# Kernel optimization log

Hardware: AMD Instinct MI355X
Metric: run time of the kernel (lower is better)

## Reference

```python
import jax, jax.numpy as jnp
import numpy as np

# Per-type input feature dims (NODE_DIM values); max dim = 128 = padded width of x.
NODE_DIMS = np.array([16, 32, 64, 128, 64, 32, 16, 128], dtype=np.int32)
N_TYPES = 8
MAX_DIM = 128
FEAT = 256          # node_feature_dim
N_GRAPHS = 100000   # batch_size; one node of each type per graph


def setup_inputs() -> dict:
    key = jax.random.key(0)
    k1, k2, k3 = jax.random.split(key, 3)
    num_nodes = N_GRAPHS * N_TYPES
    x = jax.random.normal(k1, (num_nodes, MAX_DIM), dtype=jnp.float32)
    # Per-type Linear weights, padded to MAX_DIM on the input axis.
    W = jax.random.normal(k2, (N_TYPES, FEAT, MAX_DIM), dtype=jnp.float32) * 0.05
    b = jax.random.normal(k3, (N_TYPES, FEAT), dtype=jnp.float32) * 0.05
    return {"x": x, "W": W, "b": b}


def reference(x, W, b):
    # Node n = g*N_TYPES + k is the type-k node of graph g (the gather index
    # ptr[b] + node_name.index(k) in the original). Dropout is eval-mode (identity).
    # Mask weight columns beyond each type's true input dim: equivalent to
    # slicing x[:, :NODE_DIM[k]] before the per-type Linear.
    mask = (jnp.arange(MAX_DIM)[None, None, :] < jnp.asarray(NODE_DIMS)[:, None, None]).astype(x.dtype)  # [T,1,D]
    W_eff = W * mask  # [T,F,D]
    xg = x.reshape(N_GRAPHS, N_TYPES, MAX_DIM)  # [G,T,D]
    y = jnp.einsum("gtd,tfd->gtf", xg, W_eff) + b[None, :, :]  # [G,T,F]
    return y.reshape(N_GRAPHS * N_TYPES, FEAT)
```

## Files before the change

kernel.cpp:

```cpp
#include <hip/hip_runtime.h>
#include <hip/hip_bf16.h>

#define N_GRAPHS 100000
#define NTYPES 8
#define MAXD 128
#define FEAT 256
#define ROWS 64

typedef __attribute__((ext_vector_type(8))) short short8;
typedef __attribute__((ext_vector_type(4))) float f32x4;
typedef __attribute__((ext_vector_type(4))) unsigned uint4v;

constexpr int DIMS[NTYPES] = {16, 32, 64, 128, 64, 32, 16, 128};

__device__ __forceinline__ unsigned f2bf_u(float f) {
    unsigned u = __builtin_bit_cast(unsigned, f);
    return (u + 0x7fffu + ((u >> 16) & 1u)) >> 16;
}
__device__ __forceinline__ unsigned cvt2(float lo, float hi) {
    return f2bf_u(lo) | (f2bf_u(hi) << 16);
}
__device__ __forceinline__ short8 cvt8(f32x4 a, f32x4 b) {
    uint4v u;
    u.x = cvt2(a.x, a.y); u.y = cvt2(a.z, a.w);
    u.z = cvt2(b.x, b.y); u.w = cvt2(b.z, b.w);
    return __builtin_bit_cast(short8, u);
}

__global__ __launch_bounds__(256)
void prepack_w(const float* __restrict__ W, short8* __restrict__ wp)
{
    const int idx  = blockIdx.x * 256 + threadIdx.x;
    const int c16  = idx & 15;
    const int cgrp = (idx >> 4) & 3;
    const int ks   = (idx >> 6) & 3;
    const int nt   = (idx >> 8) & 3;
    const int wb   = (idx >> 10) & 3;
    const int t    = (idx >> 12) & 7;
    const int col  = wb * 64 + nt * 16 + c16;
    const int k    = ks * 32 + cgrp * 8;
    const int dim  = 16 << ((0x30123210u >> (4 * t)) & 0xf);
    const float* src = W + ((size_t)t * FEAT + col) * MAXD + k;
    f32x4 a = *(const f32x4*)src;
    f32x4 b = *(const f32x4*)(src + 4);
    #pragma unroll
    for (int j = 0; j < 4; ++j) {
        if (k + j     >= dim) a[j] = 0.f;
        if (k + 4 + j >= dim) b[j] = 0.f;
    }
    wp[idx] = cvt8(a, b);
}

template<int K32>
__device__ __forceinline__ void stage_tile(const float* __restrict__ x, int grow0, int t,
                                           unsigned short (* __restrict__ As)[136], int tid)
{
    constexpr int TPR    = K32 / 8;
    constexpr int RPP    = 256 / TPR;
    constexpr int PASSES = ROWS / RPP;
    const int rloc = tid / TPR;
    const int kg   = tid % TPR;
    #pragma unroll
    for (int p = 0; p < PASSES; ++p) {
        const int i = p * RPP + rloc;
        int g = grow0 + i;
        if (g >= N_GRAPHS) g = N_GRAPHS - 1;
        const float* rp = x + ((size_t)g * NTYPES + t) * MAXD + kg * 8;
        f32x4 v0 = __builtin_nontemporal_load((const f32x4*)rp);
        f32x4 v1 = __builtin_nontemporal_load((const f32x4*)rp + 1);
        *(short8*)&As[i][kg * 8] = cvt8(v0, v1);
    }
}

template<int T, bool PRE>
__device__ __forceinline__ void type_step(const float* __restrict__ x,
                                          const float* __restrict__ W,
                                          const float* __restrict__ bias_g,
                                          float* __restrict__ out,
                                          const short8* __restrict__ wp,
                                          unsigned short (* __restrict__ As)[ROWS][136],
                                          int grow0, int tid, bool full)
{
    constexpr int DIM = DIMS[T];
    constexpr int KS  = (DIM + 31) / 32;
    const int lane = tid & 63, wave = tid >> 6;
    const int cgrp = lane >> 4, c16 = lane & 15;
    const int n0   = wave * 64;

    short8 Bf[KS][4];
    float  bias[4];
    #pragma unroll
    for (int nt = 0; nt < 4; ++nt) {
        bias[nt] = bias_g[T * FEAT + n0 + nt * 16 + c16];
        if constexpr (PRE) {
            #pragma unroll
            for (int ks = 0; ks < KS; ++ks)
                Bf[ks][nt] = wp[((((T * 4 + wave) * 4 + nt) * 4 + ks) * 4 + cgrp) * 16 + c16];
        } else {
            const int col = n0 + nt * 16 + c16;
            #pragma unroll
            for (int ks = 0; ks < KS; ++ks) {
                const int k = ks * 32 + cgrp * 8;
                const float* wpf = W + ((size_t)T * FEAT + col) * MAXD + k;
                f32x4 w0 = *(const f32x4*)wpf;
                f32x4 w1 = *(const f32x4*)(wpf + 4);
                #pragma unroll
                for (int j = 0; j < 4; ++j) {
                    if (k + j     >= DIM) w0[j] = 0.f;
                    if (k + 4 + j >= DIM) w1[j] = 0.f;
                }
                Bf[ks][nt] = cvt8(w0, w1);
            }
        }
    }

    __syncthreads();

    if constexpr (T + 1 < NTYPES)
        stage_tile<((DIMS[T + 1] + 31) / 32) * 32>(x, grow0, T + 1, As[(T + 1) & 1], tid);

    const unsigned short (* __restrict__ A)[136] = As[T & 1];
    #pragma unroll
    for (int ms = 0; ms < ROWS / 16; ++ms) {
        short8 a[KS];
        #pragma unroll
        for (int ks = 0; ks < KS; ++ks)
            a[ks] = *(const short8*)&A[ms * 16 + c16][ks * 32 + cgrp * 8];

        f32x4 acc[4] = {{0,0,0,0},{0,0,0,0},{0,0,0,0},{0,0,0,0}};
        #pragma unroll
        for (int ks = 0; ks < KS; ++ks) {
            #pragma unroll
            for (int nt = 0; nt < 4; ++nt)
                acc[nt] = __builtin_amdgcn_mfma_f32_16x16x32_bf16(a[ks], Bf[ks][nt], acc[nt], 0, 0, 0);
        }

        if (full) {
            #pragma unroll
            for (int nt = 0; nt < 4; ++nt) {
                const int col = n0 + nt * 16 + c16;
                #pragma unroll
                for (int r = 0; r < 4; ++r) {
                    const int g = grow0 + ms * 16 + cgrp * 4 + r;
                    __builtin_nontemporal_store(acc[nt][r] + bias[nt],
                        &out[((size_t)g * NTYPES + T) * FEAT + col]);
                }
            }
        } else {
            #pragma unroll
            for (int nt = 0; nt < 4; ++nt) {
                const int col = n0 + nt * 16 + c16;
                #pragma unroll
                for (int r = 0; r < 4; ++r) {
                    const int g = grow0 + ms * 16 + cgrp * 4 + r;
                    if (g < N_GRAPHS)
                        __builtin_nontemporal_store(acc[nt][r] + bias[nt],
                            &out[((size_t)g * NTYPES + T) * FEAT + col]);
                }
            }
        }
    }

    if constexpr (T + 1 < NTYPES)
        type_step<T + 1, PRE>(x, W, bias_g, out, wp, As, grow0, tid, full);
}

template<bool PRE>
__global__ __launch_bounds__(256, 4)
void node_enc_fused(const float* __restrict__ x, const float* __restrict__ W,
                    const float* __restrict__ bias_g, float* __restrict__ out,
                    const short8* __restrict__ wp)
{
    __shared__ __align__(16) unsigned short As[2][ROWS][136];
    const int tid   = threadIdx.x;
    const int grow0 = blockIdx.x * ROWS;
    const bool full = (grow0 + ROWS <= N_GRAPHS);

    stage_tile<((DIMS[0] + 31) / 32) * 32>(x, grow0, 0, As[0], tid);
    type_step<0, PRE>(x, W, bias_g, out, wp, As, grow0, tid, full);
}

extern "C" void kernel_launch(void* const* d_in, const int* in_sizes, int n_in,
                              void* d_out, int out_size, void* d_ws, size_t ws_size,
                              hipStream_t stream)
{
    const float* x = (const float*)d_in[0];
    const float* W = (const float*)d_in[1];
    const float* b = (const float*)d_in[2];
    float* out = (float*)d_out;

    const int chunks = (N_GRAPHS + ROWS - 1) / ROWS;
    const size_t wp_bytes = (size_t)NTYPES * 4 * 4 * 4 * 4 * 16 * sizeof(short8);

    if (ws_size >= wp_bytes) {
        short8* wp = (short8*)d_ws;
        prepack_w<<<128, 256, 0, stream>>>(W, wp);
        node_enc_fused<true><<<chunks, 256, 0, stream>>>(x, W, b, out, wp);
    } else {
        node_enc_fused<false><<<chunks, 256, 0, stream>>>(x, W, b, out, nullptr);
    }
}
```

Before: 305.0 us.

## Restructure encoder into 1024-thread blocks with all-type resident weights

Each of 16 waves now owns a 16-column feature slice and keeps bf16 weight fragments for all eight types in registers, loaded once per block. Per-graph valid input columns of all types are staged together in LDS for 16-graph slabs, double-buffered across 8 slabs per block. This removes repeated per-type weight loads and per-type synchronisation, at the cost of a large block size with register pressure under a 4-block launch bound and fewer blocks overall.

```diff
diff --git a/kernel.cpp b/kernel.cpp
--- a/kernel.cpp
+++ b/kernel.cpp
@@ -1,17 +1,21 @@
 #include <hip/hip_runtime.h>
-#include <hip/hip_bf16.h>
 
 #define N_GRAPHS 100000
 #define NTYPES 8
 #define MAXD 128
 #define FEAT 256
-#define ROWS 64
+#define SPB 8
+#define GPB (16 * SPB)
 
 typedef __attribute__((ext_vector_type(8))) short short8;
 typedef __attribute__((ext_vector_type(4))) float f32x4;
 typedef __attribute__((ext_vector_type(4))) unsigned uint4v;
 
-constexpr int DIMS[NTYPES] = {16, 32, 64, 128, 64, 32, 16, 128};
+constexpr int KSN[NTYPES]   = {1, 1, 2, 4, 2, 1, 1, 4};
+constexpr int KSOFF[NTYPES] = {0, 1, 2, 4, 8, 10, 11, 12};
+constexpr int OFFC[NTYPES]  = {0, 32, 64, 128, 256, 320, 352, 384};
+#define KTOT 16
+#define LDA 524
 
 __device__ __forceinline__ unsigned f2bf_u(float f) {
     unsigned u = __builtin_bit_cast(unsigned, f);
@@ -34,10 +38,9 @@
     const int c16  = idx & 15;
     const int cgrp = (idx >> 4) & 3;
     const int ks   = (idx >> 6) & 3;
-    const int nt   = (idx >> 8) & 3;
-    const int wb   = (idx >> 10) & 3;
+    const int ct   = (idx >> 8) & 15;
     const int t    = (idx >> 12) & 7;
-    const int col  = wb * 64 + nt * 16 + c16;
+    const int col  = ct * 16 + c16;
     const int k    = ks * 32 + cgrp * 8;
     const int dim  = 16 << ((0x30123210u >> (4 * t)) & 0xf);
     const float* src = W + ((size_t)t * FEAT + col) * MAXD + k;
@@ -51,133 +54,104 @@
     wp[idx] = cvt8(a, b);
 }
 
-template<int K32>
-__device__ __forceinline__ void stage_tile(const float* __restrict__ x, int grow0, int t,
-                                           unsigned short (* __restrict__ As)[136], int tid)
+__device__ __forceinline__ void stage16(const float* __restrict__ x, int gs,
+                                        unsigned short (* __restrict__ As)[LDA], int tid)
 {
-    constexpr int TPR    = K32 / 8;
-    constexpr int RPP    = 256 / TPR;
-    constexpr int PASSES = ROWS / RPP;
-    const int rloc = tid / TPR;
-    const int kg   = tid % TPR;
-    #pragma unroll
-    for (int p = 0; p < PASSES; ++p) {
-        const int i = p * RPP + rloc;
-        int g = grow0 + i;
-        if (g >= N_GRAPHS) g = N_GRAPHS - 1;
-        const float* rp = x + ((size_t)g * NTYPES + t) * MAXD + kg * 8;
-        f32x4 v0 = __builtin_nontemporal_load((const f32x4*)rp);
-        f32x4 v1 = __builtin_nontemporal_load((const f32x4*)rp + 1);
-        *(short8*)&As[i][kg * 8] = cvt8(v0, v1);
-    }
+    const int row = tid >> 6;
+    const int c8  = tid & 63;
+    const int t = (c8 >= 4) + (c8 >= 8) + (c8 >= 16) + (c8 >= 32) +
+                  (c8 >= 40) + (c8 >= 44) + (c8 >= 48);
+    const int off8 = c8 < 4 ? 0 : c8 < 8 ? 4 : c8 < 16 ? 8 : c8 < 32 ? 16 :
+                     c8 < 40 ? 32 : c8 < 44 ? 40 : c8 < 48 ? 44 : 48;
+    const int k8 = c8 - off8;
+    const float* rp = x + (((size_t)(gs + row)) * NTYPES + t) * MAXD + k8 * 8;
+    f32x4 v0 = __builtin_nontemporal_load((const f32x4*)rp);
+    f32x4 v1 = __builtin_nontemporal_load((const f32x4*)rp + 1);
+    *(short8*)&As[row][c8 * 8] = cvt8(v0, v1);
 }
 
 template<int T, bool PRE>
-__device__ __forceinline__ void type_step(const float* __restrict__ x,
-                                          const float* __restrict__ W,
-                                          const float* __restrict__ bias_g,
-                                          float* __restrict__ out,
-                                          const short8* __restrict__ wp,
-                                          unsigned short (* __restrict__ As)[ROWS][136],
-                                          int grow0, int tid, bool full)
+__device__ __forceinline__ void load_bf(short8* __restrict__ Bf,
+                                        const short8* __restrict__ wp,
+                                        const float* __restrict__ W,
+                                        int wave, int cgrp, int c16)
 {
-    constexpr int DIM = DIMS[T];
-    constexpr int KS  = (DIM + 31) / 32;
-    const int lane = tid & 63, wave = tid >> 6;
-    const int cgrp = lane >> 4, c16 = lane & 15;
-    const int n0   = wave * 64;
-
-    short8 Bf[KS][4];
-    float  bias[4];
-    #pragma unroll
-    for (int nt = 0; nt < 4; ++nt) {
-        bias[nt] = bias_g[T * FEAT + n0 + nt * 16 + c16];
-        if constexpr (PRE) {
+    if constexpr (PRE) {
+        #pragma unroll
+        for (int ks = 0; ks < KSN[T]; ++ks)
+            Bf[KSOFF[T] + ks] = wp[(((T * 16 + wave) * 4 + ks) * 4 + cgrp) * 16 + c16];
+    } else {
+        constexpr int DIM = (T==0||T==6) ? 16 : (T==1||T==5) ? 32 : (T==2||T==4) ? 64 : 128;
+        const int col = wave * 16 + c16;
+        #pragma unroll
+        for (int ks = 0; ks < KSN[T]; ++ks) {
+            const int k = ks * 32 + cgrp * 8;
+            const float* wf = W + ((size_t)T * FEAT + col) * MAXD + k;
+            f32x4 a = *(const f32x4*)wf;
+            f32x4 b = *(const f32x4*)(wf + 4);
             #pragma unroll
-            for (int ks = 0; ks < KS; ++ks)
-                Bf[ks][nt] = wp[((((T * 4 + wave) * 4 + nt) * 4 + ks) * 4 + cgrp) * 16 + c16];
-        } else {
-            const int col = n0 + nt * 16 + c16;
-            #pragma unroll
-            for (int ks = 0; ks < KS; ++ks) {
-                const int k = ks * 32 + cgrp * 8;
-                const float* wpf = W + ((size_t)T * FEAT + col) * MAXD + k;
-                f32x4 w0 = *(const f32x4*)wpf;
-                f32x4 w1 = *(const f32x4*)(wpf + 4);
-                #pragma unroll
-                for (int j = 0; j < 4; ++j) {
-                    if (k + j     >= DIM) w0[j] = 0.f;
-                    if (k + 4 + j >= DIM) w1[j] = 0.f;
-                }
-                Bf[ks][nt] = cvt8(w0, w1);
+            for (int j = 0; j < 4; ++j) {
+                if (k + j     >= DIM) a[j] = 0.f;
+                if (k + 4 + j >= DIM) b[j] = 0.f;
             }
+            Bf[KSOFF[T] + ks] = cvt8(a, b);
         }
     }
+    if constexpr (T + 1 < NTYPES) load_bf<T + 1, PRE>(Bf, wp, W, wave, cgrp, c16);
+}
 
-    __syncthreads();
-
-    if constexpr (T + 1 < NTYPES)
-        stage_tile<((DIMS[T + 1] + 31) / 32) * 32>(x, grow0, T + 1, As[(T + 1) & 1], tid);
-
-    const unsigned short (* __restrict__ A)[136] = As[T & 1];
+template<int T>
+__device__ __forceinline__ void compute_types(const short8* __restrict__ Bf,
+                                              const unsigned short (* __restrict__ A)[LDA],
+                                              float* __restrict__ out,
+                                              const float* __restrict__ bias_g,
+                                              int gs, int wave, int cgrp, int c16)
+{
+    f32x4 acc = {0.f, 0.f, 0.f, 0.f};
     #pragma unroll
-    for (int ms = 0; ms < ROWS / 16; ++ms) {
-        short8 a[KS];
-        #pragma unroll
-        for (int ks = 0; ks < KS; ++ks)
-            a[ks] = *(const short8*)&A[ms * 16 + c16][ks * 32 + cgrp * 8];
-
-        f32x4 acc[4] = {{0,0,0,0},{0,0,0,0},{0,0,0,0},{0,0,0,0}};
-        #pragma unroll
-        for (int ks = 0; ks < KS; ++ks) {
-            #pragma unroll
-            for (int nt = 0; nt < 4; ++nt)
-                acc[nt] = __builtin_amdgcn_mfma_f32_16x16x32_bf16(a[ks], Bf[ks][nt], acc[nt], 0, 0, 0);
-        }
-
-        if (full) {
-            #pragma unroll
-            for (int nt = 0; nt < 4; ++nt) {
-                const int col = n0 + nt * 16 + c16;
-                #pragma unroll
-                for (int r = 0; r < 4; ++r) {
-                    const int g = grow0 + ms * 16 + cgrp * 4 + r;
-                    __builtin_nontemporal_store(acc[nt][r] + bias[nt],
-                        &out[((size_t)g * NTYPES + T) * FEAT + col]);
-                }
-            }
-        } else {
-            #pragma unroll
-            for (int nt = 0; nt < 4; ++nt) {
-                const int col = n0 + nt * 16 + c16;
-                #pragma unroll
-                for (int r = 0; r < 4; ++r) {
-                    const int g = grow0 + ms * 16 + cgrp * 4 + r;
-                    if (g < N_GRAPHS)
-                        __builtin_nontemporal_store(acc[nt][r] + bias[nt],
-                            &out[((size_t)g * NTYPES + T) * FEAT + col]);
-                }
-            }
-        }
+    for (int ks = 0; ks < KSN[T]; ++ks) {
+        short8 a = *(const short8*)&A[c16][OFFC[T] + ks * 32 + cgrp * 8];
+        acc = __builtin_amdgcn_mfma_f32_16x16x32_bf16(a, Bf[KSOFF[T] + ks], acc, 0, 0, 0);
     }
-
-    if constexpr (T + 1 < NTYPES)
-        type_step<T + 1, PRE>(x, W, bias_g, out, wp, As, grow0, tid, full);
+    const int col = wave * 16 + c16;
+    const float bv = bias_g[T * FEAT + col];
+    #pragma unroll
+    for (int r = 0; r < 4; ++r) {
+        const int g = gs + cgrp * 4 + r;
+        __builtin_nontemporal_store(acc[r] + bv,
+            &out[((size_t)g * NTYPES + T) * FEAT + col]);
+    }
+    if constexpr (T + 1 < NTYPES) compute_types<T + 1>(Bf, A, out, bias_g, gs, wave, cgrp, c16);
 }
 
 template<bool PRE>
-__global__ __launch_bounds__(256, 4)
-void node_enc_fused(const float* __restrict__ x, const float* __restrict__ W,
-                    const float* __restrict__ bias_g, float* __restrict__ out,
-                    const short8* __restrict__ wp)
+__global__ __launch_bounds__(1024, 4)
+void node_enc(const float* __restrict__ x, const short8* __restrict__ wp,
+              const float* __restrict__ W, const float* __restrict__ bias_g,
+              float* __restrict__ out)
 {
-    __shared__ __align__(16) unsigned short As[2][ROWS][136];
-    const int tid   = threadIdx.x;
-    const int grow0 = blockIdx.x * ROWS;
-    const bool full = (grow0 + ROWS <= N_GRAPHS);
+    __shared__ __align__(16) unsigned short As[2][16][LDA];
+    const int tid  = threadIdx.x;
+    const int lane = tid & 63;
+    const int wave = tid >> 6;
+    const int cgrp = lane >> 4;
+    const int c16  = lane & 15;
+    const int g0   = blockIdx.x * GPB;
 
-    stage_tile<((DIMS[0] + 31) / 32) * 32>(x, grow0, 0, As[0], tid);
-    type_step<0, PRE>(x, W, bias_g, out, wp, As, grow0, tid, full);
+    short8 Bf[KTOT];
+    load_bf<0, PRE>(Bf, wp, W, wave, cgrp, c16);
+
+    stage16(x, g0, As[0], tid);
+
+    for (int s = 0; s < SPB; ++s) {
+        const int gs = g0 + s * 16;
+        if (gs >= N_GRAPHS) break;
+        __syncthreads();
+        const int gn = gs + 16;
+        if (s + 1 < SPB && gn < N_GRAPHS)
+            stage16(x, gn, As[(s + 1) & 1], tid);
+        compute_types<0>(Bf, As[s & 1], out, bias_g, gs, wave, cgrp, c16);
+    }
 }
 
 extern "C" void kernel_launch(void* const* d_in, const int* in_sizes, int n_in,
@@ -189,14 +163,14 @@
     const float* b = (const float*)d_in[2];
     float* out = (float*)d_out;
 
-    const int chunks = (N_GRAPHS + ROWS - 1) / ROWS;
-    const size_t wp_bytes = (size_t)NTYPES * 4 * 4 * 4 * 4 * 16 * sizeof(short8);
+    const int grid = (N_GRAPHS + GPB - 1) / GPB;
+    const size_t wp_bytes = (size_t)32768 * sizeof(short8);
 
     if (ws_size >= wp_bytes) {
         short8* wp = (short8*)d_ws;
         prepack_w<<<128, 256, 0, stream>>>(W, wp);
-        node_enc_fused<true><<<chunks, 256, 0, stream>>>(x, W, b, out, wp);
+        node_enc<true><<<grid, 1024, 0, stream>>>(x, wp, W, b, out);
     } else {
-        node_enc_fused<false><<<chunks, 256, 0, stream>>>(x, W, b, out, nullptr);
+        node_enc<false><<<grid, 1024, 0, stream>>>(x, nullptr, W, b, out);
     }
 }
```

After: 328.0 us. 1.08x slower.
